# Kernel tuning notes

Hardware: AMD Instinct MI355X
Metric: run time of the kernel (lower is better)

Reference implementation:

```python
import jax, jax.numpy as jnp
import numpy as np

USER_NUM = 100000
ITEM_NUM = 50000
N = USER_NUM + ITEM_NUM
EMB = 64
NNZ = 8000000
N_LAYERS = 3
GAMMA = 0.5
EPS = 1e-12


def setup_inputs() -> dict:
    key = jax.random.key(0)
    k1, k2, k3, k4, k5 = jax.random.split(key, 5)
    user_emb = jax.random.normal(k1, (USER_NUM, EMB), dtype=jnp.float32) * 0.1
    item_emb = jax.random.normal(k2, (ITEM_NUM, EMB), dtype=jnp.float32) * 0.1
    adj_rows = jax.random.randint(k3, (NNZ,), 0, N, dtype=jnp.int32)
    adj_cols = jax.random.randint(k4, (NNZ,), 0, N, dtype=jnp.int32)
    # normalized adjacency values are small positive numbers
    adj_vals = jax.random.uniform(k5, (NNZ,), dtype=jnp.float32) * 0.02
    return {"user_emb": user_emb, "item_emb": item_emb,
            "adj_rows": adj_rows, "adj_cols": adj_cols, "adj_vals": adj_vals}


def _spmm(rows, cols, vals, x):
    # y[r] += vals * x[c]  over COO nonzeros; x: [N, d]
    msgs = vals[:, None] * x[cols]          # [nnz, d]
    return jax.ops.segment_sum(msgs, rows, num_segments=N)


def reference(user_emb, item_emb, adj_rows, adj_cols, adj_vals):
    ego = jnp.concatenate([user_emb, item_emb], axis=0)  # [N, d]
    embs_zero = ego
    prop_sum = jnp.zeros_like(ego)
    for _ in range(N_LAYERS):
        norm = jnp.linalg.norm(ego, axis=1) + EPS        # row L2 norm, [N]
        ego = ego / norm[:, None]
        ego = _spmm(adj_rows, adj_cols, adj_vals, ego)
        prop_sum = prop_sum + ego
    embs_prop = prop_sum / N_LAYERS
    light_out = GAMMA * embs_zero + (1.0 - GAMMA) * embs_prop
    return light_out[:USER_NUM], light_out[USER_NUM:]
```

## Files before the change

### kernel.cpp

```cpp
#include <hip/hip_runtime.h>

#define USER_NUM 100000
#define ITEM_NUM 50000
#define NTOT     (USER_NUM + ITEM_NUM)
#define EMB      64
#define GAMMA    0.5f
#define NLAYERS  3
#define EPS      1e-12f

#define SCAN_CHUNK 256
#define NCHUNKS    ((NTOT + SCAN_CHUNK - 1) / SCAN_CHUNK)

__device__ __forceinline__ unsigned short f2bf(float f) {
    unsigned u = __float_as_uint(f);
    u = (u + 0x7FFFu + ((u >> 16) & 1u)) >> 16;
    return (unsigned short)u;
}
__device__ __forceinline__ float bf2f(unsigned short h) {
    return __uint_as_float((unsigned)h << 16);
}

__global__ void init_kernel(const float* __restrict__ user_emb,
                            const float* __restrict__ item_emb,
                            unsigned short* __restrict__ Xh,
                            float* __restrict__ out) {
    int tid = blockIdx.x * blockDim.x + threadIdx.x;
    int row = tid >> 4;
    if (row >= NTOT) return;
    int l = tid & 15;
    const float* src = (row < USER_NUM)
        ? user_emb + (size_t)row * EMB
        : item_emb + (size_t)(row - USER_NUM) * EMB;
    float4 v = reinterpret_cast<const float4*>(src)[l];
    float4 o = v; o.x *= GAMMA; o.y *= GAMMA; o.z *= GAMMA; o.w *= GAMMA;
    reinterpret_cast<float4*>(out)[(size_t)row * 16 + l] = o;
    float ss = v.x * v.x + v.y * v.y + v.z * v.z + v.w * v.w;
    ss += __shfl_xor(ss, 1);
    ss += __shfl_xor(ss, 2);
    ss += __shfl_xor(ss, 4);
    ss += __shfl_xor(ss, 8);
    float inv = 1.0f / (sqrtf(ss) + EPS);
    ushort4 h;
    h.x = f2bf(v.x * inv); h.y = f2bf(v.y * inv);
    h.z = f2bf(v.z * inv); h.w = f2bf(v.w * inv);
    reinterpret_cast<ushort4*>(Xh)[(size_t)row * 16 + l] = h;
}

__global__ void hist4_kernel(const int* __restrict__ rows,
                             int* __restrict__ counts, int nnz) {
    int tid = blockIdx.x * blockDim.x + threadIdx.x;
    int stride = gridDim.x * blockDim.x;
    int nnz4 = nnz >> 2;
    for (int i = tid; i < nnz4; i += stride) {
        int4 r4 = reinterpret_cast<const int4*>(rows)[i];
        atomicAdd(&counts[r4.x], 1);
        atomicAdd(&counts[r4.y], 1);
        atomicAdd(&counts[r4.z], 1);
        atomicAdd(&counts[r4.w], 1);
    }
    if (tid == 0)
        for (int i = nnz4 << 2; i < nnz; ++i) atomicAdd(&counts[rows[i]], 1);
}

__global__ void scan_sums_kernel(const int* __restrict__ counts,
                                 int* __restrict__ chunk_sums) {
    __shared__ int sdata[SCAN_CHUNK];
    int idx = blockIdx.x * SCAN_CHUNK + threadIdx.x;
    int v = (idx < NTOT) ? counts[idx] : 0;
    sdata[threadIdx.x] = v;
    __syncthreads();
    for (int off = SCAN_CHUNK / 2; off > 0; off >>= 1) {
        if (threadIdx.x < off) sdata[threadIdx.x] += sdata[threadIdx.x + off];
        __syncthreads();
    }
    if (threadIdx.x == 0) chunk_sums[blockIdx.x] = sdata[0];
}

__global__ void scan_offsets_kernel(int* __restrict__ chunk_sums,
                                    int* __restrict__ row_ptr) {
    if (threadIdx.x == 0 && blockIdx.x == 0) {
        int running = 0;
        for (int b = 0; b < NCHUNKS; ++b) {
            int t = chunk_sums[b];
            chunk_sums[b] = running;
            running += t;
        }
        row_ptr[NTOT] = running;
    }
}

__global__ void scan_write_kernel(const int* __restrict__ counts,
                                  const int* __restrict__ chunk_sums,
                                  int* __restrict__ row_ptr,
                                  int* __restrict__ cursor) {
    __shared__ int temp[SCAN_CHUNK];
    int idx = blockIdx.x * SCAN_CHUNK + threadIdx.x;
    int v = (idx < NTOT) ? counts[idx] : 0;
    temp[threadIdx.x] = v;
    __syncthreads();
    for (int off = 1; off < SCAN_CHUNK; off <<= 1) {
        int t = (threadIdx.x >= off) ? temp[threadIdx.x - off] : 0;
        __syncthreads();
        temp[threadIdx.x] += t;
        __syncthreads();
    }
    if (idx < NTOT) {
        int excl = temp[threadIdx.x] - v + chunk_sums[blockIdx.x];
        row_ptr[idx] = excl;
        cursor[idx]  = excl;
    }
}

__global__ void build_kernel(const int* __restrict__ rows,
                             const int* __restrict__ cols,
                             const float* __restrict__ vals,
                             int* __restrict__ cursor,
                             int2* __restrict__ cv, int nnz) {
    int stride = gridDim.x * blockDim.x;
    for (int i = blockIdx.x * blockDim.x + threadIdx.x; i < nnz; i += stride) {
        int r = rows[i];
        int pos = atomicAdd(&cursor[r], 1);
        cv[pos] = make_int2(cols[i], __float_as_int(vals[i]));
    }
}

template <int WRITE_NORM>
__global__ void spmm_csr_kernel(const int* __restrict__ row_ptr,
                                const int2* __restrict__ cv,
                                const unsigned short* __restrict__ Xh,
                                unsigned short* __restrict__ Yh,
                                float* __restrict__ out,
                                float scale) {
    int wave = (blockIdx.x * blockDim.x + threadIdx.x) >> 6;
    if (wave >= NTOT) return;
    int lane = threadIdx.x & 63;
    int start = __builtin_amdgcn_readfirstlane(row_ptr[wave]);
    int end   = __builtin_amdgcn_readfirstlane(row_ptr[wave + 1]);
    int n = end - start;
    const int2* p = cv + start;

    float acc = 0.0f;
    int k = 0;
    for (; k + 8 <= n; k += 8) {
        int2 c0 = p[k + 0], c1 = p[k + 1], c2 = p[k + 2], c3 = p[k + 3];
        int2 c4 = p[k + 4], c5 = p[k + 5], c6 = p[k + 6], c7 = p[k + 7];
        float x0 = bf2f(Xh[(size_t)c0.x * EMB + lane]);
        float x1 = bf2f(Xh[(size_t)c1.x * EMB + lane]);
        float x2 = bf2f(Xh[(size_t)c2.x * EMB + lane]);
        float x3 = bf2f(Xh[(size_t)c3.x * EMB + lane]);
        float x4 = bf2f(Xh[(size_t)c4.x * EMB + lane]);
        float x5 = bf2f(Xh[(size_t)c5.x * EMB + lane]);
        float x6 = bf2f(Xh[(size_t)c6.x * EMB + lane]);
        float x7 = bf2f(Xh[(size_t)c7.x * EMB + lane]);
        acc += __int_as_float(c0.y) * x0;
        acc += __int_as_float(c1.y) * x1;
        acc += __int_as_float(c2.y) * x2;
        acc += __int_as_float(c3.y) * x3;
        acc += __int_as_float(c4.y) * x4;
        acc += __int_as_float(c5.y) * x5;
        acc += __int_as_float(c6.y) * x6;
        acc += __int_as_float(c7.y) * x7;
    }
    for (; k + 4 <= n; k += 4) {
        int2 c0 = p[k + 0], c1 = p[k + 1], c2 = p[k + 2], c3 = p[k + 3];
        float x0 = bf2f(Xh[(size_t)c0.x * EMB + lane]);
        float x1 = bf2f(Xh[(size_t)c1.x * EMB + lane]);
        float x2 = bf2f(Xh[(size_t)c2.x * EMB + lane]);
        float x3 = bf2f(Xh[(size_t)c3.x * EMB + lane]);
        acc += __int_as_float(c0.y) * x0;
        acc += __int_as_float(c1.y) * x1;
        acc += __int_as_float(c2.y) * x2;
        acc += __int_as_float(c3.y) * x3;
    }
    for (; k < n; ++k) {
        int2 c0 = p[k];
        acc += __int_as_float(c0.y) * bf2f(Xh[(size_t)c0.x * EMB + lane]);
    }

    size_t o = (size_t)wave * EMB + lane;
    out[o] += scale * acc;
    if (WRITE_NORM) {
        float ss = acc * acc;
        ss += __shfl_xor(ss, 1);
        ss += __shfl_xor(ss, 2);
        ss += __shfl_xor(ss, 4);
        ss += __shfl_xor(ss, 8);
        ss += __shfl_xor(ss, 16);
        ss += __shfl_xor(ss, 32);
        float inv = 1.0f / (sqrtf(ss) + EPS);
        Yh[o] = f2bf(acc * inv);
    }
}


__global__ void scale_copy_kernel(const float* __restrict__ src,
                                  float* __restrict__ dst, float a, int n4) {
    int stride = gridDim.x * blockDim.x;
    for (int i = blockIdx.x * blockDim.x + threadIdx.x; i < n4; i += stride) {
        float4 v = reinterpret_cast<const float4*>(src)[i];
        v.x *= a; v.y *= a; v.z *= a; v.w *= a;
        reinterpret_cast<float4*>(dst)[i] = v;
    }
}

__global__ void normalize_kernel(const float* __restrict__ src,
                                 float* __restrict__ dst, int nrows) {
    int tid = blockIdx.x * blockDim.x + threadIdx.x;
    int row = tid >> 4;
    if (row >= nrows) return;
    int l = tid & 15;
    float4 v = reinterpret_cast<const float4*>(src)[(size_t)row * 16 + l];
    float ss = v.x * v.x + v.y * v.y + v.z * v.z + v.w * v.w;
    ss += __shfl_xor(ss, 1);
    ss += __shfl_xor(ss, 2);
    ss += __shfl_xor(ss, 4);
    ss += __shfl_xor(ss, 8);
    float inv = 1.0f / (sqrtf(ss) + EPS);
    v.x *= inv; v.y *= inv; v.z *= inv; v.w *= inv;
    reinterpret_cast<float4*>(dst)[(size_t)row * 16 + l] = v;
}

__global__ void spmm_scatter_kernel(const int* __restrict__ rows,
                                    const int* __restrict__ cols,
                                    const float* __restrict__ vals,
                                    const float* __restrict__ x,
                                    float* __restrict__ y, int nnz) {
    int lane = threadIdx.x & 63;
    int wave = (blockIdx.x * blockDim.x + threadIdx.x) >> 6;
    int nw   = (gridDim.x * blockDim.x) >> 6;
    for (int i = wave; i < nnz; i += nw) {
        int   r = rows[i];
        int   c = cols[i];
        float v = vals[i];
        atomicAdd(&y[(size_t)r * EMB + lane], v * x[(size_t)c * EMB + lane]);
    }
}

__global__ void axpy_kernel(const float* __restrict__ x,
                            float* __restrict__ out, float a, int n4) {
    int stride = gridDim.x * blockDim.x;
    for (int i = blockIdx.x * blockDim.x + threadIdx.x; i < n4; i += stride) {
        float4 v = reinterpret_cast<const float4*>(x)[i];
        float4 o = reinterpret_cast<float4*>(out)[i];
        o.x += a * v.x; o.y += a * v.y; o.z += a * v.z; o.w += a * v.w;
        reinterpret_cast<float4*>(out)[i] = o;
    }
}


extern "C" void kernel_launch(void* const* d_in, const int* in_sizes, int n_in,
                              void* d_out, int out_size, void* d_ws, size_t ws_size,
                              hipStream_t stream) {
    const float* user_emb = (const float*)d_in[0];
    const float* item_emb = (const float*)d_in[1];
    const int*   rows     = (const int*)d_in[2];
    const int*   cols     = (const int*)d_in[3];
    const float* vals     = (const float*)d_in[4];
    const int    nnz      = in_sizes[2];

    float* out = (float*)d_out;
    const int TOTAL = NTOT * EMB;
    const float layer_scale = (1.0f - GAMMA) / NLAYERS;
    const int SPMM_BLOCKS = (NTOT * 64 + 255) / 256;

    size_t need = (size_t)TOTAL * 2 * 2
                + (size_t)nnz * 8
                + (size_t)(NTOT + 1) * 4
                + (size_t)NTOT * 4
                + (size_t)NCHUNKS * 4
                + 1024;

    if (ws_size >= need) {
        char* p = (char*)d_ws;
        unsigned short* Xh = (unsigned short*)p;  p += (size_t)TOTAL * 2;
        unsigned short* Yh = (unsigned short*)p;  p += (size_t)TOTAL * 2;
        int2* cv           = (int2*)p;            p += (size_t)nnz * 8;
        int*  row_ptr      = (int*)p;             p += (size_t)(NTOT + 1) * 4;
        int*  cursor       = (int*)p;             p += (size_t)NTOT * 4;
        int*  chunks       = (int*)p;

        init_kernel<<<(NTOT * 16 + 255) / 256, 256, 0, stream>>>(
            user_emb, item_emb, Xh, out);

        hipMemsetAsync(cursor, 0, (size_t)NTOT * 4, stream);
        hist4_kernel<<<2048, 256, 0, stream>>>(rows, cursor, nnz);
        scan_sums_kernel<<<NCHUNKS, SCAN_CHUNK, 0, stream>>>(cursor, chunks);
        scan_offsets_kernel<<<1, 64, 0, stream>>>(chunks, row_ptr);
        scan_write_kernel<<<NCHUNKS, SCAN_CHUNK, 0, stream>>>(cursor, chunks,
                                                              row_ptr, cursor);
        build_kernel<<<4096, 256, 0, stream>>>(rows, cols, vals, cursor, cv, nnz);

        spmm_csr_kernel<1><<<SPMM_BLOCKS, 256, 0, stream>>>(
            row_ptr, cv, Xh, Yh, out, layer_scale);
        spmm_csr_kernel<1><<<SPMM_BLOCKS, 256, 0, stream>>>(
            row_ptr, cv, Yh, Xh, out, layer_scale);
        spmm_csr_kernel<0><<<SPMM_BLOCKS, 256, 0, stream>>>(
            row_ptr, cv, Xh, Yh, out, layer_scale);
        return;
    }

    float* A = (float*)d_ws;
    float* B = A + (size_t)TOTAL;
    const int T4 = TOTAL / 4;

    scale_copy_kernel<<<2048, 256, 0, stream>>>(user_emb, out, GAMMA,
                                                USER_NUM * EMB / 4);
    scale_copy_kernel<<<2048, 256, 0, stream>>>(item_emb, out + (size_t)USER_NUM * EMB,
                                                GAMMA, ITEM_NUM * EMB / 4);
    normalize_kernel<<<(USER_NUM * 16 + 255) / 256, 256, 0, stream>>>(
        user_emb, A, USER_NUM);
    normalize_kernel<<<(ITEM_NUM * 16 + 255) / 256, 256, 0, stream>>>(
        item_emb, A + (size_t)USER_NUM * EMB, ITEM_NUM);

    for (int layer = 0; layer < NLAYERS; ++layer) {
        if (layer > 0)
            normalize_kernel<<<(NTOT * 16 + 255) / 256, 256, 0, stream>>>(B, A, NTOT);
        hipMemsetAsync(B, 0, (size_t)TOTAL * sizeof(float), stream);
        spmm_scatter_kernel<<<8192, 256, 0, stream>>>(rows, cols, vals, A, B, nnz);
        axpy_kernel<<<2048, 256, 0, stream>>>(B, out, layer_scale, T4);
    }
}
```

Baseline: 1.226 ms.

## Partition CSR build by XCD row windows and vectorize SpMM gathers per half-wave

The CSR build is split into 8 row windows balanced by nonzero count, and each block handles only the window matching blockIdx&7. The intent is to keep atomics and scattered writes for a given row range within one XCD's L2 instead of bouncing across dies. The SpMM kernel now has each half-wave process alternate nonzeros with 32-bit loads of two bf16 values, then combines the halves with a cross-half shuffle, which halves gather instructions per row. The cost is that every block reads the whole rows array, which is 8x the row-index traffic, and this relies on the assumption that blocks are dispatched round-robin across XCDs.

```diff
diff --git a/kernel.cpp b/kernel.cpp
--- a/kernel.cpp
+++ b/kernel.cpp
@@ -111,16 +111,64 @@
     }
 }
 
-__global__ void build_kernel(const int* __restrict__ rows,
-                             const int* __restrict__ cols,
-                             const float* __restrict__ vals,
-                             int* __restrict__ cursor,
-                             int2* __restrict__ cv, int nnz) {
-    int stride = gridDim.x * blockDim.x;
-    for (int i = blockIdx.x * blockDim.x + threadIdx.x; i < nnz; i += stride) {
-        int r = rows[i];
-        int pos = atomicAdd(&cursor[r], 1);
-        cv[pos] = make_int2(cols[i], __float_as_int(vals[i]));
+__global__ void winbounds_kernel(const int* __restrict__ row_ptr,
+                                 int* __restrict__ rb, int nnz) {
+    int w = threadIdx.x;
+    if (w > 8) return;
+    if (w == 0) { rb[0] = 0; return; }
+    if (w == 8) { rb[8] = NTOT; return; }
+    int target = (int)(((long long)nnz * w) >> 3);
+    int lo = 0, hi = NTOT;
+    while (lo < hi) {
+        int mid = (lo + hi) >> 1;
+        if (row_ptr[mid] < target) lo = mid + 1; else hi = mid;
+    }
+    rb[w] = lo;
+}
+
+__global__ void build_xcd_kernel(const int* __restrict__ rows,
+                                 const int* __restrict__ cols,
+                                 const float* __restrict__ vals,
+                                 int* __restrict__ cursor,
+                                 const int* __restrict__ rb,
+                                 int2* __restrict__ cv, int nnz) {
+    __shared__ int srb[8];
+    if (threadIdx.x < 8) srb[threadIdx.x] = rb[threadIdx.x];
+    __syncthreads();
+    const int b1 = srb[1], b2 = srb[2], b3 = srb[3], b4 = srb[4];
+    const int b5 = srb[5], b6 = srb[6], b7 = srb[7];
+    const int win = blockIdx.x & 7;
+
+    int i4      = (blockIdx.x >> 3) * blockDim.x + threadIdx.x;
+    int stride4 = (gridDim.x >> 3) * blockDim.x;
+    int nnz4    = nnz >> 2;
+    for (; i4 < nnz4; i4 += stride4) {
+        int4 r4 = reinterpret_cast<const int4*>(rows)[i4];
+        int rr[4] = {r4.x, r4.y, r4.z, r4.w};
+#pragma unroll
+        for (int j = 0; j < 4; ++j) {
+            int r = rr[j];
+            int w = (r >= b1) + (r >= b2) + (r >= b3) + (r >= b4)
+                  + (r >= b5) + (r >= b6) + (r >= b7);
+            if (w == win) {
+                int i = (i4 << 2) + j;
+                int   c = cols[i];
+                float v = vals[i];
+                int pos = atomicAdd(&cursor[r], 1);
+                cv[pos] = make_int2(c, __float_as_int(v));
+            }
+        }
+    }
+    if ((blockIdx.x >> 3) == 0 && threadIdx.x == 0) {
+        for (int i = nnz4 << 2; i < nnz; ++i) {
+            int r = rows[i];
+            int w = (r >= b1) + (r >= b2) + (r >= b3) + (r >= b4)
+                  + (r >= b5) + (r >= b6) + (r >= b7);
+            if (w == win) {
+                int pos = atomicAdd(&cursor[r], 1);
+                cv[pos] = make_int2(cols[i], __float_as_int(vals[i]));
+            }
+        }
     }
 }
 
@@ -134,61 +182,80 @@
     int wave = (blockIdx.x * blockDim.x + threadIdx.x) >> 6;
     if (wave >= NTOT) return;
     int lane = threadIdx.x & 63;
+    int half = lane >> 5;
+    int l    = lane & 31;
     int start = __builtin_amdgcn_readfirstlane(row_ptr[wave]);
     int end   = __builtin_amdgcn_readfirstlane(row_ptr[wave + 1]);
     int n = end - start;
     const int2* p = cv + start;
 
-    float acc = 0.0f;
+    float accx = 0.0f, accy = 0.0f;
     int k = 0;
     for (; k + 8 <= n; k += 8) {
-        int2 c0 = p[k + 0], c1 = p[k + 1], c2 = p[k + 2], c3 = p[k + 3];
-        int2 c4 = p[k + 4], c5 = p[k + 5], c6 = p[k + 6], c7 = p[k + 7];
-        float x0 = bf2f(Xh[(size_t)c0.x * EMB + lane]);
-        float x1 = bf2f(Xh[(size_t)c1.x * EMB + lane]);
-        float x2 = bf2f(Xh[(size_t)c2.x * EMB + lane]);
-        float x3 = bf2f(Xh[(size_t)c3.x * EMB + lane]);
-        float x4 = bf2f(Xh[(size_t)c4.x * EMB + lane]);
-        float x5 = bf2f(Xh[(size_t)c5.x * EMB + lane]);
-        float x6 = bf2f(Xh[(size_t)c6.x * EMB + lane]);
-        float x7 = bf2f(Xh[(size_t)c7.x * EMB + lane]);
-        acc += __int_as_float(c0.y) * x0;
-        acc += __int_as_float(c1.y) * x1;
-        acc += __int_as_float(c2.y) * x2;
-        acc += __int_as_float(c3.y) * x3;
-        acc += __int_as_float(c4.y) * x4;
-        acc += __int_as_float(c5.y) * x5;
-        acc += __int_as_float(c6.y) * x6;
-        acc += __int_as_float(c7.y) * x7;
-    }
-    for (; k + 4 <= n; k += 4) {
-        int2 c0 = p[k + 0], c1 = p[k + 1], c2 = p[k + 2], c3 = p[k + 3];
-        float x0 = bf2f(Xh[(size_t)c0.x * EMB + lane]);
-        float x1 = bf2f(Xh[(size_t)c1.x * EMB + lane]);
-        float x2 = bf2f(Xh[(size_t)c2.x * EMB + lane]);
-        float x3 = bf2f(Xh[(size_t)c3.x * EMB + lane]);
-        acc += __int_as_float(c0.y) * x0;
-        acc += __int_as_float(c1.y) * x1;
-        acc += __int_as_float(c2.y) * x2;
-        acc += __int_as_float(c3.y) * x3;
-    }
-    for (; k < n; ++k) {
+        int2 c0 = p[k + 0 + half];
+        int2 c1 = p[k + 2 + half];
+        int2 c2 = p[k + 4 + half];
+        int2 c3 = p[k + 6 + half];
+        unsigned x0 = *reinterpret_cast<const unsigned*>(
+            Xh + (size_t)c0.x * EMB + 2 * l);
+        unsigned x1 = *reinterpret_cast<const unsigned*>(
+            Xh + (size_t)c1.x * EMB + 2 * l);
+        unsigned x2 = *reinterpret_cast<const unsigned*>(
+            Xh + (size_t)c2.x * EMB + 2 * l);
+        unsigned x3 = *reinterpret_cast<const unsigned*>(
+            Xh + (size_t)c3.x * EMB + 2 * l);
+        float v0 = __int_as_float(c0.y), v1 = __int_as_float(c1.y);
+        float v2 = __int_as_float(c2.y), v3 = __int_as_float(c3.y);
+        accx += v0 * bf2f((unsigned short)(x0 & 0xFFFF));
+        accy += v0 * bf2f((unsigned short)(x0 >> 16));
+        accx += v1 * bf2f((unsigned short)(x1 & 0xFFFF));
+        accy += v1 * bf2f((unsigned short)(x1 >> 16));
+        accx += v2 * bf2f((unsigned short)(x2 & 0xFFFF));
+        accy += v2 * bf2f((unsigned short)(x2 >> 16));
+        accx += v3 * bf2f((unsigned short)(x3 & 0xFFFF));
+        accy += v3 * bf2f((unsigned short)(x3 >> 16));
+    }
+    for (; k + 2 <= n; k += 2) {
+        int2 c0 = p[k + half];
+        unsigned x0 = *reinterpret_cast<const unsigned*>(
+            Xh + (size_t)c0.x * EMB + 2 * l);
+        float v0 = __int_as_float(c0.y);
+        accx += v0 * bf2f((unsigned short)(x0 & 0xFFFF));
+        accy += v0 * bf2f((unsigned short)(x0 >> 16));
+    }
+    if (k < n && half == 0) {
         int2 c0 = p[k];
-        acc += __int_as_float(c0.y) * bf2f(Xh[(size_t)c0.x * EMB + lane]);
-    }
-
-    size_t o = (size_t)wave * EMB + lane;
-    out[o] += scale * acc;
+        unsigned x0 = *reinterpret_cast<const unsigned*>(
+            Xh + (size_t)c0.x * EMB + 2 * l);
+        float v0 = __int_as_float(c0.y);
+        accx += v0 * bf2f((unsigned short)(x0 & 0xFFFF));
+        accy += v0 * bf2f((unsigned short)(x0 >> 16));
+    }
+
+    accx += __shfl_xor(accx, 32);
+    accy += __shfl_xor(accy, 32);
+
+    size_t o = (size_t)wave * EMB + 2 * l;
+    if (half == 0) {
+        float2 prev = *reinterpret_cast<float2*>(&out[o]);
+        prev.x += scale * accx;
+        prev.y += scale * accy;
+        *reinterpret_cast<float2*>(&out[o]) = prev;
+    }
     if (WRITE_NORM) {
-        float ss = acc * acc;
+        float ss = accx * accx + accy * accy;
         ss += __shfl_xor(ss, 1);
         ss += __shfl_xor(ss, 2);
         ss += __shfl_xor(ss, 4);
         ss += __shfl_xor(ss, 8);
         ss += __shfl_xor(ss, 16);
-        ss += __shfl_xor(ss, 32);
         float inv = 1.0f / (sqrtf(ss) + EPS);
-        Yh[o] = f2bf(acc * inv);
+        if (half == 0) {
+            ushort2 h;
+            h.x = f2bf(accx * inv);
+            h.y = f2bf(accy * inv);
+            *reinterpret_cast<ushort2*>(&Yh[o]) = h;
+        }
     }
 }
 
@@ -268,6 +335,7 @@
                 + (size_t)(NTOT + 1) * 4
                 + (size_t)NTOT * 4
                 + (size_t)NCHUNKS * 4
+                + 64
                 + 1024;
 
     if (ws_size >= need) {
@@ -277,7 +345,8 @@
         int2* cv           = (int2*)p;            p += (size_t)nnz * 8;
         int*  row_ptr      = (int*)p;             p += (size_t)(NTOT + 1) * 4;
         int*  cursor       = (int*)p;             p += (size_t)NTOT * 4;
-        int*  chunks       = (int*)p;
+        int*  chunks       = (int*)p;             p += (size_t)NCHUNKS * 4;
+        int*  rb           = (int*)p;
 
         init_kernel<<<(NTOT * 16 + 255) / 256, 256, 0, stream>>>(
             user_emb, item_emb, Xh, out);
@@ -288,7 +357,9 @@
         scan_offsets_kernel<<<1, 64, 0, stream>>>(chunks, row_ptr);
         scan_write_kernel<<<NCHUNKS, SCAN_CHUNK, 0, stream>>>(cursor, chunks,
                                                               row_ptr, cursor);
-        build_kernel<<<4096, 256, 0, stream>>>(rows, cols, vals, cursor, cv, nnz);
+        winbounds_kernel<<<1, 16, 0, stream>>>(row_ptr, rb, nnz);
+        build_xcd_kernel<<<2048, 256, 0, stream>>>(rows, cols, vals, cursor,
+                                                   rb, cv, nnz);
 
         spmm_csr_kernel<1><<<SPMM_BLOCKS, 256, 0, stream>>>(
             row_ptr, cv, Xh, Yh, out, layer_scale);
```

New measurement: 1.311 ms. 1.07x slower.

## Partition CSR build scatter by row window per XCD to localize atomics

Applied to the files above, without the earlier changes.

Replaces the flat COO-to-CSR scatter with a kernel where each block handles one of eight row windows (chosen by blockIdx mod 8, matching round-robin XCD dispatch), with window bounds found by a small binary-search kernel over row_ptr. Each block reads all row indices but only scatters the entries in its window, so cursor atomics and cv writes for a given row range stay within one XCD's L2. The cost is reading the rows array eight times overall and more per-thread branching, and it depends on the block-to-XCD mapping holding.

```diff
diff --git a/kernel.cpp b/kernel.cpp
--- a/kernel.cpp
+++ b/kernel.cpp
@@ -98,7 +98,7 @@
     int v = (idx < NTOT) ? counts[idx] : 0;
     temp[threadIdx.x] = v;
     __syncthreads();
-    for (int off = 1; off < SCAN_CHUNK; off <<= 1) {
+    for (int off = 1; off < 256; off <<= 1) {
         int t = (threadIdx.x >= off) ? temp[threadIdx.x - off] : 0;
         __syncthreads();
         temp[threadIdx.x] += t;
@@ -111,16 +111,64 @@
     }
 }
 
-__global__ void build_kernel(const int* __restrict__ rows,
-                             const int* __restrict__ cols,
-                             const float* __restrict__ vals,
-                             int* __restrict__ cursor,
-                             int2* __restrict__ cv, int nnz) {
-    int stride = gridDim.x * blockDim.x;
-    for (int i = blockIdx.x * blockDim.x + threadIdx.x; i < nnz; i += stride) {
-        int r = rows[i];
-        int pos = atomicAdd(&cursor[r], 1);
-        cv[pos] = make_int2(cols[i], __float_as_int(vals[i]));
+__global__ void winbounds_kernel(const int* __restrict__ row_ptr,
+                                 int* __restrict__ rb, int nnz) {
+    int w = threadIdx.x;
+    if (w > 8) return;
+    if (w == 0) { rb[0] = 0; return; }
+    if (w == 8) { rb[8] = NTOT; return; }
+    int target = (int)(((long long)nnz * w) >> 3);
+    int lo = 0, hi = NTOT;
+    while (lo < hi) {
+        int mid = (lo + hi) >> 1;
+        if (row_ptr[mid] < target) lo = mid + 1; else hi = mid;
+    }
+    rb[w] = lo;
+}
+
+__global__ void build_xcd_kernel(const int* __restrict__ rows,
+                                 const int* __restrict__ cols,
+                                 const float* __restrict__ vals,
+                                 int* __restrict__ cursor,
+                                 const int* __restrict__ rb,
+                                 int2* __restrict__ cv, int nnz) {
+    __shared__ int srb[8];
+    if (threadIdx.x < 8) srb[threadIdx.x] = rb[threadIdx.x];
+    __syncthreads();
+    const int b1 = srb[1], b2 = srb[2], b3 = srb[3], b4 = srb[4];
+    const int b5 = srb[5], b6 = srb[6], b7 = srb[7];
+    const int win = blockIdx.x & 7;
+
+    int i4      = (blockIdx.x >> 3) * blockDim.x + threadIdx.x;
+    int stride4 = (gridDim.x >> 3) * blockDim.x;
+    int nnz4    = nnz >> 2;
+    for (; i4 < nnz4; i4 += stride4) {
+        int4 r4 = reinterpret_cast<const int4*>(rows)[i4];
+        int rr[4] = {r4.x, r4.y, r4.z, r4.w};
+#pragma unroll
+        for (int j = 0; j < 4; ++j) {
+            int r = rr[j];
+            int w = (r >= b1) + (r >= b2) + (r >= b3) + (r >= b4)
+                  + (r >= b5) + (r >= b6) + (r >= b7);
+            if (w == win) {
+                int i = (i4 << 2) + j;
+                int   c = cols[i];
+                float v = vals[i];
+                int pos = atomicAdd(&cursor[r], 1);
+                cv[pos] = make_int2(c, __float_as_int(v));
+            }
+        }
+    }
+    if ((blockIdx.x >> 3) == 0 && threadIdx.x == 0) {
+        for (int i = nnz4 << 2; i < nnz; ++i) {
+            int r = rows[i];
+            int w = (r >= b1) + (r >= b2) + (r >= b3) + (r >= b4)
+                  + (r >= b5) + (r >= b6) + (r >= b7);
+            if (w == win) {
+                int pos = atomicAdd(&cursor[r], 1);
+                cv[pos] = make_int2(cols[i], __float_as_int(vals[i]));
+            }
+        }
     }
 }
 
@@ -268,6 +316,7 @@
                 + (size_t)(NTOT + 1) * 4
                 + (size_t)NTOT * 4
                 + (size_t)NCHUNKS * 4
+                + 64
                 + 1024;
 
     if (ws_size >= need) {
@@ -277,7 +326,8 @@
         int2* cv           = (int2*)p;            p += (size_t)nnz * 8;
         int*  row_ptr      = (int*)p;             p += (size_t)(NTOT + 1) * 4;
         int*  cursor       = (int*)p;             p += (size_t)NTOT * 4;
-        int*  chunks       = (int*)p;
+        int*  chunks       = (int*)p;             p += (size_t)NCHUNKS * 4;
+        int*  rb           = (int*)p;
 
         init_kernel<<<(NTOT * 16 + 255) / 256, 256, 0, stream>>>(
             user_emb, item_emb, Xh, out);
@@ -288,7 +338,9 @@
         scan_offsets_kernel<<<1, 64, 0, stream>>>(chunks, row_ptr);
         scan_write_kernel<<<NCHUNKS, SCAN_CHUNK, 0, stream>>>(cursor, chunks,
                                                               row_ptr, cursor);
-        build_kernel<<<4096, 256, 0, stream>>>(rows, cols, vals, cursor, cv, nnz);
+        winbounds_kernel<<<1, 16, 0, stream>>>(row_ptr, rb, nnz);
+        build_xcd_kernel<<<2048, 256, 0, stream>>>(rows, cols, vals, cursor,
+                                                   rb, cv, nnz);
 
         spmm_csr_kernel<1><<<SPMM_BLOCKS, 256, 0, stream>>>(
             row_ptr, cv, Xh, Yh, out, layer_scale);
```

New measurement: 1.233 ms. About the same (+0.6%).
